# Optimization experiments

Measured on AMD Instinct MI355X. Metric: run time of the kernel, lower is better.

The kernel has to match this reference:

```python
import jax, jax.numpy as jnp
import numpy as np

B, H, E, V = 128, 1024, 1024, 40000
L, S, A = 256, 10, 10
L_S, L_A = 1.0, 1.0  # s_copy_lambda / a_copy_lambda
NEG = -1e24


def setup_inputs():
    key = jax.random.key(0)
    ks = jax.random.split(key, 32)
    n = lambda i, shape: jax.random.normal(ks[i], shape, dtype=jnp.float32)
    p = lambda i, shape: jax.random.normal(ks[i], shape, dtype=jnp.float32) * 0.02
    rnn_in = 3 * E + H  # embed + history ctx (H) + state ctx (E) + action ctx (E)
    return {
        "inp": n(0, (B, 1, E)),
        "hidden": n(1, (1, B, H)),
        "hs_vectors": n(2, (B, L, H)),
        "state_gumbel_prob": jax.random.uniform(ks[3], (B, S, V), dtype=jnp.float32),
        "state_gumbel_embed": n(4, (B, S, E)),
        "action_gumbel_prob": jax.random.uniform(ks[5], (B, A, V), dtype=jnp.float32),
        "action_gumbel_embed": n(6, (B, A, E)),
        "history_lens": jax.random.randint(ks[7], (B,), 1, L + 1),
        "history_word_indices": jax.random.randint(ks[8], (B, L), 0, V),
        # history word mlp-attention
        "Wq_hist": p(9, (H, H)), "bq_hist": jnp.zeros((H,), jnp.float32),
        "Wm_hist": p(10, (H, H)), "v_hist": p(11, (H,)),
        # init_s_attn / init_a_attn (query H, memory E)
        "Wq_s": p(12, (H, H)), "bq_s": jnp.zeros((H,), jnp.float32),
        "Wm_s": p(13, (E, H)), "v_s": p(14, (H,)),
        "Wq_a": p(15, (H, H)), "bq_a": jnp.zeros((H,), jnp.float32),
        "Wm_a": p(16, (E, H)), "v_a": p(17, (H,)),
        # sparse_copy_attn (memory E+1)
        "Wq_sc": p(18, (H, H)), "bq_sc": jnp.zeros((H,), jnp.float32),
        "Wm_sc": p(19, (E + 1, H)), "v_sc": p(20, (H,)),
        # GRU (torch layout: [3H, in], gate order r,z,n)
        "W_ih": p(21, (3 * H, rnn_in)), "W_hh": p(22, (3 * H, H)),
        "b_ih": jnp.zeros((3 * H,), jnp.float32), "b_hh": jnp.zeros((3 * H,), jnp.float32),
        # output projection
        "W_out": p(23, (H, V)), "b_out": jnp.zeros((V,), jnp.float32),
    }


def _mlp_scores(q, mem, Wq, bq, Wm, v):
    # q: [B,1,H], mem: [B,L,M] -> additive-attention logits [B,1,L]
    t = jnp.tanh((q @ Wq + bq) + (mem @ Wm))  # [B,L,H]
    return (t @ v)[:, None, :]


def reference(inp, hidden, hs_vectors, state_gumbel_prob, state_gumbel_embed,
              action_gumbel_prob, action_gumbel_embed, history_lens,
              history_word_indices, Wq_hist, bq_hist, Wm_hist, v_hist,
              Wq_s, bq_s, Wm_s, v_s, Wq_a, bq_a, Wm_a, v_a,
              Wq_sc, bq_sc, Wm_sc, v_sc, W_ih, W_hh, b_ih, b_hh, W_out, b_out):
    q0 = jnp.transpose(hidden, (1, 0, 2))  # [B,1,H]
    # --- history word attention (masked mlp attention) ---
    hist_scores = _mlp_scores(q0, hs_vectors, Wq_hist, bq_hist, Wm_hist, v_hist)
    valid = jnp.arange(L)[None, None, :] < history_lens[:, None, None]
    hist_scores = jnp.where(valid, hist_scores, NEG)
    c_his = jax.nn.softmax(hist_scores, axis=-1) @ hs_vectors  # [B,1,H]
    # --- init_consult over state / action gumbel embeddings ---
    sw = jax.nn.softmax(_mlp_scores(q0, state_gumbel_embed, Wq_s, bq_s, Wm_s, v_s), axis=-1)
    c_state = sw @ state_gumbel_embed  # [B,1,E]
    aw = jax.nn.softmax(_mlp_scores(q0, action_gumbel_embed, Wq_a, bq_a, Wm_a, v_a), axis=-1)
    c_action = aw @ action_gumbel_embed  # [B,1,E]
    x = jnp.concatenate([inp, c_his, c_state, c_action], axis=-1)[:, 0, :]  # [B,3E+H]
    # --- single-step GRU cell (torch semantics, gate order r,z,n) ---
    h0 = hidden[0]
    gi = x @ W_ih.T + b_ih
    gh = h0 @ W_hh.T + b_hh
    ir, iz, inn = jnp.split(gi, 3, axis=-1)
    hr, hz, hn = jnp.split(gh, 3, axis=-1)
    r = jax.nn.sigmoid(ir + hr)
    z = jax.nn.sigmoid(iz + hz)
    nact = jnp.tanh(inn + r * hn)
    h_new = (1.0 - z) * nact + z * h0  # [B,H]
    # --- vocab logits + copy logits, joint softmax ---
    gene_logits = h_new @ W_out + b_out  # [B,V]
    cq = h_new[:, None, :]
    hs_logits = jnp.einsum('bqh,blh->bql', cq, hs_vectors)[:, 0, :]  # dot attn, [B,L]
    s_tag = jnp.zeros((B, S, 1), jnp.float32)
    a_tag = jnp.ones((B, A, 1), jnp.float32)
    st_logits = _mlp_scores(cq, jnp.concatenate([state_gumbel_embed, s_tag], -1), Wq_sc, bq_sc, Wm_sc, v_sc)[:, 0, :]
    ac_logits = _mlp_scores(cq, jnp.concatenate([action_gumbel_embed, a_tag], -1), Wq_sc, bq_sc, Wm_sc, v_sc)[:, 0, :]
    all_logits = jnp.concatenate([gene_logits, hs_logits, st_logits, ac_logits], axis=-1)
    wp = jax.nn.softmax(all_logits, axis=-1)  # [B, V+L+S+A]
    gene_p = wp[:, :V]
    hs_w = wp[:, V:V + L]
    st_w = wp[:, V + L:V + L + S]
    ac_w = wp[:, V + L + S:]
    # --- copy-distribution mixing ---
    scp = jnp.einsum('bs,bsv->bv', st_w, state_gumbel_prob)
    acp = jnp.einsum('ba,bav->bv', ac_w, action_gumbel_prob)
    gene_p = gene_p + L_S * scp + L_A * acp
    copy_p = jnp.zeros((B, V), jnp.float32).at[jnp.arange(B)[:, None], history_word_indices].add(hs_w)
    out = jnp.log(gene_p + copy_p)[:, None, :]  # [B,1,V]
    return out, h_new[None]
```

## Files before the change

kernel.cpp:

```cpp
#include <hip/hip_runtime.h>
#include <stdint.h>

typedef __attribute__((ext_vector_type(4))) float f32x4;
typedef __attribute__((ext_vector_type(2))) unsigned int u32x2;
typedef __attribute__((ext_vector_type(4))) unsigned int u32x4;
typedef __attribute__((ext_vector_type(8))) short bf16x8;

#define BV (128*40000)

__device__ __forceinline__ unsigned rne_bf16(float f) {
    unsigned x = __float_as_uint(f);
    return ((x + 0x7FFFu + ((x >> 16) & 1u)) >> 16) & 0xFFFFu;
}
__device__ __forceinline__ unsigned pack2(float a, float b) {
    return rne_bf16(a) | (rne_bf16(b) << 16);
}
__device__ __forceinline__ float bf2f(unsigned u) {
    return __uint_as_float((u & 0xFFFFu) << 16);
}
__device__ __forceinline__ float sigm(float x) { return 1.0f / (1.0f + expf(-x)); }

__device__ __forceinline__ void gload16(const void* g, void* l) {
    __builtin_amdgcn_global_load_lds(
        (const __attribute__((address_space(1))) unsigned*)g,
        (__attribute__((address_space(3))) unsigned*)l, 16, 0, 0);
}

template<int EPI>
__device__ __forceinline__ void mgemm(
    const unsigned short* __restrict__ A, const unsigned short* __restrict__ Bt,
    float* __restrict__ out, const float* __restrict__ rb,
    const float* __restrict__ cb1, const float* __restrict__ cb2,
    const float* __restrict__ vvec,
    int m0, int n0, int kb, int ke, int ldk, int ldc, int rpb)
{
    __shared__ unsigned short As[2][4096];
    __shared__ unsigned short Bs[2][4096];
    const int t = threadIdx.x, lane = t & 63, wv = t >> 6;
    const int l16 = lane & 15, lq = lane >> 4;
    const int wm = wv >> 1, wn = wv & 1;

    const int srow = lane >> 2, scol = (lane & 3) << 3;
    const unsigned short* gA0 = A + (size_t)(m0 + (wv << 4) + srow) * ldk + kb + scol;
    const unsigned short* gA1 = gA0 + (size_t)64 * ldk;
    const unsigned short* gB0 = Bt + (size_t)(n0 + (wv << 4) + srow) * ldk + kb + scol;
    const unsigned short* gB1 = gB0 + (size_t)64 * ldk;
    unsigned short* lA0 = &As[0][wv << 9];
    unsigned short* lA1 = &As[0][(wv + 4) << 9];
    unsigned short* lB0 = &Bs[0][wv << 9];
    unsigned short* lB1 = &Bs[0][(wv + 4) << 9];

    f32x4 acc[4][4];
#pragma unroll
    for (int i = 0; i < 4; ++i)
#pragma unroll
        for (int j = 0; j < 4; ++j) acc[i][j] = (f32x4){0.f, 0.f, 0.f, 0.f};

    const int NS = (ke - kb) >> 5;
    gload16(gA0, lA0); gload16(gA1, lA1);
    gload16(gB0, lB0); gload16(gB1, lB1);

    for (int s = 0; s < NS; ++s) {
        __syncthreads();
        if (s + 1 < NS) {
            const int nb = (s + 1) & 1, ko = (s + 1) << 5;
            gload16(gA0 + ko, lA0 + (nb << 12)); gload16(gA1 + ko, lA1 + (nb << 12));
            gload16(gB0 + ko, lB0 + (nb << 12)); gload16(gB1 + ko, lB1 + (nb << 12));
        }
        const unsigned short* ab = As[s & 1];
        const unsigned short* bb = Bs[s & 1];
        bf16x8 af[4], bfv[4];
#pragma unroll
        for (int i = 0; i < 4; ++i)
            af[i] = *(const bf16x8*)(ab + (((wm << 6) + (i << 4) + l16) << 5) + (lq << 3));
#pragma unroll
        for (int i = 0; i < 4; ++i)
            bfv[i] = *(const bf16x8*)(bb + (((wn << 6) + (i << 4) + l16) << 5) + (lq << 3));
#pragma unroll
        for (int mf = 0; mf < 4; ++mf)
#pragma unroll
            for (int nf = 0; nf < 4; ++nf)
                acc[mf][nf] = __builtin_amdgcn_mfma_f32_16x16x32_bf16(af[mf], bfv[nf], acc[mf][nf], 0, 0, 0);
    }

    if (EPI == 1) {
#pragma unroll
        for (int mf = 0; mf < 4; ++mf) {
#pragma unroll
            for (int r = 0; r < 4; ++r) {
                int gr = m0 + (wm << 6) + (mf << 4) + (lq << 2) + r;
                const float* rbp = rb + (size_t)(gr / rpb) * 1024;
                float s = 0.0f;
#pragma unroll
                for (int nf = 0; nf < 4; ++nf) {
                    int gc = n0 + (wn << 6) + (nf << 4) + l16;
                    float xv = acc[mf][nf][r] + rbp[gc] + cb1[gc];
                    if (cb2) xv += cb2[gc];
                    s += tanhf(xv) * vvec[gc];
                }
#pragma unroll
                for (int msk = 1; msk < 16; msk <<= 1) s += __shfl_xor(s, msk, 64);
                if (l16 == 0) atomicAdd(&out[gr], s);
            }
        }
    } else {
#pragma unroll
        for (int mf = 0; mf < 4; ++mf) {
            int gr0 = m0 + (wm << 6) + (mf << 4) + (lq << 2);
#pragma unroll
            for (int nf = 0; nf < 4; ++nf) {
                int gc = n0 + (wn << 6) + (nf << 4) + l16;
#pragma unroll
                for (int r = 0; r < 4; ++r)
                    atomicAdd(&out[(size_t)(gr0 + r) * ldc + gc], acc[mf][nf][r]);
            }
        }
    }
}

__global__ __launch_bounds__(256) void k_hist2(
    const unsigned short* hs, const unsigned short* WmhT, const int* lens,
    const float* qh_h, const float* bq, const float* v, float* hsc) {
    int h = blockIdx.x;
    int p = h & 255, n = h >> 8;
    int b = p >> 1, l0 = (p & 1) << 7;
    if (lens[b] <= l0) return;
    mgemm<1>(hs, WmhT, hsc, qh_h, bq, nullptr, v, p << 7, n << 7, 0, 1024, 1024, 0, 256);
}

__global__ __launch_bounds__(256) void k_att3(
    const unsigned short* se, const unsigned short* ae,
    const unsigned short* WmsT, const unsigned short* WmaT,
    const float* qh_s, const float* qh_a, const float* bq_s, const float* bq_a,
    const float* v_s, const float* v_a, float* stsc, float* acsc) {
    if (blockIdx.z == 0)
        mgemm<1>(se, WmsT, stsc, qh_s, bq_s, nullptr, v_s, blockIdx.y * 128, blockIdx.x * 128, 0, 1024, 1024, 0, 10);
    else
        mgemm<1>(ae, WmaT, acsc, qh_a, bq_a, nullptr, v_a, blockIdx.y * 128, blockIdx.x * 128, 0, 1024, 1024, 0, 10);
}

__global__ __launch_bounds__(256) void k_stac3(
    const unsigned short* se, const unsigned short* ae, const unsigned short* WmscT,
    const float* tagrow, const float* qsc, const float* bq_sc, const float* v_sc,
    float* stlg, float* aclg) {
    if (blockIdx.z == 0)
        mgemm<1>(se, WmscT, stlg, qsc, bq_sc, nullptr, v_sc, blockIdx.y * 128, blockIdx.x * 128, 0, 1024, 1024, 0, 10);
    else
        mgemm<1>(ae, WmscT, aclg, qsc, bq_sc, tagrow, v_sc, blockIdx.y * 128, blockIdx.x * 128, 0, 1024, 1024, 0, 10);
}

__global__ __launch_bounds__(256) void k_qh4(
    const unsigned short* q0, const unsigned short* W0, const unsigned short* W1,
    const unsigned short* W2, float* o0, float* o1, float* o2) {
    const unsigned short* W = W0; float* o = o0;
    if (blockIdx.z == 1) { W = W1; o = o1; }
    if (blockIdx.z == 2) { W = W2; o = o2; }
    int kb = blockIdx.y << 8;
    mgemm<2>(q0, W, o, nullptr, nullptr, nullptr, nullptr, 0, blockIdx.x * 128, kb, kb + 256, 1024, 1024, 1);
}

__global__ __launch_bounds__(256) void k_gigh2(
    const unsigned short* xb, const unsigned short* q0,
    const unsigned short* Wih, const unsigned short* Whh, float* gi, float* gh) {
    if (blockIdx.z == 0) {
        int kb = blockIdx.y << 9;
        mgemm<2>(xb, Wih, gi, nullptr, nullptr, nullptr, nullptr, 0, blockIdx.x * 128, kb, kb + 512, 4096, 3072, 1);
    } else {
        if (blockIdx.y >= 2) return;
        int kb = blockIdx.y << 9;
        mgemm<2>(q0, Whh, gh, nullptr, nullptr, nullptr, nullptr, 0, blockIdx.x * 128, kb, kb + 512, 1024, 3072, 1);
    }
}

__global__ __launch_bounds__(256) void k_qsc2(
    const unsigned short* hnb, const unsigned short* WqscT, float* qsc) {
    int kb = blockIdx.y << 9;
    mgemm<2>(hnb, WqscT, qsc, nullptr, nullptr, nullptr, nullptr, 0, blockIdx.x * 128, kb, kb + 512, 1024, 1024, 1);
}

__global__ __launch_bounds__(256) void k_geneKN(
    const unsigned short* __restrict__ hnb, const float* __restrict__ Wout,
    float* __restrict__ out) {
    __shared__ unsigned short As[2][4096];
    __shared__ unsigned short Bs[2][4096];
    const int t = threadIdx.x, lane = t & 63, wv = t >> 6;
    const int l16 = lane & 15, lq = lane >> 4;
    const int wm = wv >> 1, wn = wv & 1;
    const int n0 = blockIdx.x << 7;
    const int kb = blockIdx.y << 9;

    const int srow = lane >> 2, scol = (lane & 3) << 3;
    const unsigned short* gA0 = hnb + (size_t)((wv << 4) + srow) * 1024 + kb + scol;
    const unsigned short* gA1 = gA0 + (size_t)64 * 1024;
    unsigned short* lA0 = &As[0][wv << 9];
    unsigned short* lA1 = &As[0][(wv + 4) << 9];

    const int bn = t & 127, kh = t >> 7;
    const bool ok = (n0 + bn) < 40000;
    const float* gB = Wout + (size_t)(kb + kh * 16) * 40000 + (n0 + bn);

    f32x4 acc[4][4];
#pragma unroll
    for (int i = 0; i < 4; ++i)
#pragma unroll
        for (int j = 0; j < 4; ++j) acc[i][j] = (f32x4){0.f, 0.f, 0.f, 0.f};

    auto stageB = [&](int buf, int ko) {
        const float* src = gB + (size_t)ko * 40000;
        float f[16];
#pragma unroll
        for (int j = 0; j < 16; ++j) f[j] = ok ? src[(size_t)j * 40000] : 0.0f;
        u32x4* d = (u32x4*)&Bs[buf][bn * 32 + kh * 16];
        d[0] = (u32x4){pack2(f[0],f[1]), pack2(f[2],f[3]), pack2(f[4],f[5]), pack2(f[6],f[7])};
        d[1] = (u32x4){pack2(f[8],f[9]), pack2(f[10],f[11]), pack2(f[12],f[13]), pack2(f[14],f[15])};
    };

    gload16(gA0, lA0); gload16(gA1, lA1); stageB(0, 0);
    for (int s = 0; s < 16; ++s) {
        __syncthreads();
        if (s + 1 < 16) {
            const int nb = (s + 1) & 1, ko = (s + 1) << 5;
            gload16(gA0 + ko, lA0 + (nb << 12)); gload16(gA1 + ko, lA1 + (nb << 12));
            stageB(nb, ko);
        }
        const unsigned short* ab = As[s & 1];
        const unsigned short* bb = Bs[s & 1];
        bf16x8 af[4], bfv[4];
#pragma unroll
        for (int i = 0; i < 4; ++i)
            af[i] = *(const bf16x8*)(ab + (((wm << 6) + (i << 4) + l16) << 5) + (lq << 3));
#pragma unroll
        for (int i = 0; i < 4; ++i)
            bfv[i] = *(const bf16x8*)(bb + (((wn << 6) + (i << 4) + l16) << 5) + (lq << 3));
#pragma unroll
        for (int mf = 0; mf < 4; ++mf)
#pragma unroll
            for (int nf = 0; nf < 4; ++nf)
                acc[mf][nf] = __builtin_amdgcn_mfma_f32_16x16x32_bf16(af[mf], bfv[nf], acc[mf][nf], 0, 0, 0);
    }
#pragma unroll
    for (int mf = 0; mf < 4; ++mf) {
        int gr0 = (wm << 6) + (mf << 4) + (lq << 2);
#pragma unroll
        for (int nf = 0; nf < 4; ++nf) {
            int gc = n0 + (wn << 6) + (nf << 4) + l16;
            if (gc < 40000) {
#pragma unroll
                for (int r = 0; r < 4; ++r)
                    atomicAdd(&out[(size_t)(gr0 + r) * 40000 + gc], acc[mf][nf][r]);
            }
        }
    }
}

__global__ __launch_bounds__(256) void k_cvt(const float* __restrict__ in,
                                             unsigned short* __restrict__ o, int n8) {
    int i = blockIdx.x * 256 + threadIdx.x;
    if (i >= n8) return;
    const f32x4* s = (const f32x4*)in + (size_t)i * 2;
    f32x4 a = s[0], b = s[1];
    ((u32x4*)o)[i] = (u32x4){pack2(a[0],a[1]), pack2(a[2],a[3]), pack2(b[0],b[1]), pack2(b[2],b[3])};
}

struct TrArgs { const float* s[8]; unsigned short* d[8]; };
__global__ __launch_bounds__(256) void k_trcvt(TrArgs a) {
    __shared__ float tile[64][65];
    const float* in = a.s[blockIdx.z];
    unsigned short* ot = a.d[blockIdx.z];
    int k0 = blockIdx.y << 6, n0 = blockIdx.x << 6;
    int tr = threadIdx.x >> 6, tc = threadIdx.x & 63;
#pragma unroll
    for (int i = 0; i < 16; ++i) {
        int r = (i << 2) + tr;
        tile[r][tc] = in[(size_t)(k0 + r) * 1024 + n0 + tc];
    }
    __syncthreads();
#pragma unroll
    for (int i = 0; i < 16; ++i) {
        int r = (i << 2) + tr;
        ot[(size_t)(n0 + r) * 1024 + k0 + tc] = (unsigned short)rne_bf16(tile[tc][r]);
    }
}

__device__ __forceinline__ void softmax10(const float* src, float* dst) {
    float m = src[0];
    for (int i = 1; i < 10; ++i) m = fmaxf(m, src[i]);
    float z = 0.f, e[10];
    for (int i = 0; i < 10; ++i) { e[i] = expf(src[i] - m); z += e[i]; }
    float iz = 1.0f / z;
    for (int i = 0; i < 10; ++i) dst[i] = e[i] * iz;
}

__global__ __launch_bounds__(256) void k_chis(
    const float* __restrict__ scores, const int* __restrict__ lens,
    const unsigned short* __restrict__ hs, unsigned short* __restrict__ xb) {
    int b = blockIdx.x, t = threadIdx.x;
    __shared__ float w[256];
    __shared__ float red[256];
    int len = lens[b];
    float s = scores[b * 256 + t];
    bool valid = t < len;
    red[t] = valid ? s : -3.0e38f;
    __syncthreads();
    for (int st = 128; st > 0; st >>= 1) { if (t < st) red[t] = fmaxf(red[t], red[t + st]); __syncthreads(); }
    float m = red[0];
    __syncthreads();
    float e = valid ? expf(s - m) : 0.0f;
    red[t] = e;
    __syncthreads();
    for (int st = 128; st > 0; st >>= 1) { if (t < st) red[t] += red[t + st]; __syncthreads(); }
    float Z = red[0];
    __syncthreads();
    w[t] = e / Z;
    __syncthreads();
    float a0 = 0.f, a1 = 0.f, a2 = 0.f, a3 = 0.f;
    for (int l = 0; l < 256; ++l) {
        float wl = w[l];
        if (wl == 0.0f) continue;
        u32x2 u = *((const u32x2*)(hs + ((size_t)b * 256 + l) * 1024) + t);
        a0 += wl * bf2f(u[0]); a1 += wl * bf2f(u[0] >> 16);
        a2 += wl * bf2f(u[1]); a3 += wl * bf2f(u[1] >> 16);
    }
    *((u32x2*)(xb + (size_t)b * 4096 + 1024) + t) = (u32x2){pack2(a0, a1), pack2(a2, a3)};
}

__global__ __launch_bounds__(256) void k_assemble(
    const float* __restrict__ inp, const float* __restrict__ st_sc, const float* __restrict__ ac_sc,
    const unsigned short* __restrict__ se, const unsigned short* __restrict__ ae,
    unsigned short* __restrict__ xb) {
    int b = blockIdx.x, t = threadIdx.x;
    __shared__ float sw[10], aw[10];
    if (t == 0) softmax10(st_sc + b * 10, sw);
    if (t == 64) softmax10(ac_sc + b * 10, aw);
    f32x4 iv = ((const f32x4*)(inp + (size_t)b * 1024))[t];
    *((u32x2*)(xb + (size_t)b * 4096) + t) = (u32x2){pack2(iv[0], iv[1]), pack2(iv[2], iv[3])};
    __syncthreads();
    float cs0=0,cs1=0,cs2=0,cs3=0, ca0=0,ca1=0,ca2=0,ca3=0;
#pragma unroll
    for (int s = 0; s < 10; ++s) {
        u32x2 us = *((const u32x2*)(se + ((size_t)b * 10 + s) * 1024) + t);
        u32x2 ua = *((const u32x2*)(ae + ((size_t)b * 10 + s) * 1024) + t);
        float ws = sw[s], wa = aw[s];
        cs0 += ws * bf2f(us[0]); cs1 += ws * bf2f(us[0] >> 16);
        cs2 += ws * bf2f(us[1]); cs3 += ws * bf2f(us[1] >> 16);
        ca0 += wa * bf2f(ua[0]); ca1 += wa * bf2f(ua[0] >> 16);
        ca2 += wa * bf2f(ua[1]); ca3 += wa * bf2f(ua[1] >> 16);
    }
    *((u32x2*)(xb + (size_t)b * 4096 + 2048) + t) = (u32x2){pack2(cs0, cs1), pack2(cs2, cs3)};
    *((u32x2*)(xb + (size_t)b * 4096 + 3072) + t) = (u32x2){pack2(ca0, ca1), pack2(ca2, ca3)};
}

__global__ __launch_bounds__(256) void k_gru(
    const float* __restrict__ gi, const float* __restrict__ gh,
    const float* __restrict__ b_ih, const float* __restrict__ b_hh,
    const float* __restrict__ h0, float* __restrict__ hnew,
    unsigned short* __restrict__ hnb) {
    int i = blockIdx.x * 256 + threadIdx.x;
    int b = i >> 10, j = i & 1023;
    const float* gib = gi + (size_t)b * 3072;
    const float* ghb = gh + (size_t)b * 3072;
    float ir = gib[j] + b_ih[j],           hr = ghb[j] + b_hh[j];
    float iz = gib[1024 + j] + b_ih[1024 + j], hz = ghb[1024 + j] + b_hh[1024 + j];
    float in = gib[2048 + j] + b_ih[2048 + j], hn = ghb[2048 + j] + b_hh[2048 + j];
    float r = sigm(ir + hr);
    float z = sigm(iz + hz);
    float n = tanhf(in + r * hn);
    float h = (1.0f - z) * n + z * h0[i];
    hnew[i] = h;
    hnb[i] = (unsigned short)rne_bf16(h);
}

__global__ __launch_bounds__(256) void k_hsl(
    const float* __restrict__ hnew, const unsigned short* __restrict__ hs,
    float* __restrict__ out) {
    int b = blockIdx.y;
    int w = threadIdx.x >> 6, lane = threadIdx.x & 63;
    int l = blockIdx.x * 4 + w;
    const f32x4* hr = (const f32x4*)(hnew + (size_t)b * 1024);
    const u32x4* vr = (const u32x4*)(hs + ((size_t)b * 256 + l) * 1024);
    float s = 0.f;
#pragma unroll
    for (int q = 0; q < 2; ++q) {
        u32x4 u = vr[lane * 2 + q];
        f32x4 h0 = hr[lane * 4 + q * 2], h1 = hr[lane * 4 + q * 2 + 1];
        s += h0[0]*bf2f(u[0]) + h0[1]*bf2f(u[0]>>16) + h0[2]*bf2f(u[1]) + h0[3]*bf2f(u[1]>>16);
        s += h1[0]*bf2f(u[2]) + h1[1]*bf2f(u[2]>>16) + h1[2]*bf2f(u[3]) + h1[3]*bf2f(u[3]>>16);
    }
    for (int msk = 1; msk < 64; msk <<= 1) s += __shfl_xor(s, msk, 64);
    if (lane == 0) out[b * 256 + l] = s;
}

__global__ __launch_bounds__(256) void k_smstats(
    const float* __restrict__ gene, const float* __restrict__ bo,
    const float* __restrict__ hsl, const float* __restrict__ stl, const float* __restrict__ acl,
    float* __restrict__ mbuf, float* __restrict__ zbuf) {
    int b = blockIdx.x, t = threadIdx.x;
    __shared__ float red[256];
    const f32x4* g4 = (const f32x4*)(gene + (size_t)b * 40000);
    const f32x4* b4 = (const f32x4*)bo;
    float mx = -3.0e38f;
    for (int i = t; i < 10000; i += 256) {
        f32x4 q = g4[i], bb = b4[i];
        mx = fmaxf(mx, fmaxf(fmaxf(q[0]+bb[0], q[1]+bb[1]), fmaxf(q[2]+bb[2], q[3]+bb[3])));
    }
    mx = fmaxf(mx, hsl[b * 256 + t]);
    if (t < 10) mx = fmaxf(mx, fmaxf(stl[b * 10 + t], acl[b * 10 + t]));
    red[t] = mx; __syncthreads();
    for (int s = 128; s > 0; s >>= 1) { if (t < s) red[t] = fmaxf(red[t], red[t + s]); __syncthreads(); }
    float m = red[0];
    __syncthreads();
    float sum = 0.f;
    for (int i = t; i < 10000; i += 256) {
        f32x4 q = g4[i], bb = b4[i];
        sum += expf(q[0]+bb[0]-m) + expf(q[1]+bb[1]-m) + expf(q[2]+bb[2]-m) + expf(q[3]+bb[3]-m);
    }
    sum += expf(hsl[b * 256 + t] - m);
    if (t < 10) sum += expf(stl[b * 10 + t] - m) + expf(acl[b * 10 + t] - m);
    red[t] = sum; __syncthreads();
    for (int s = 128; s > 0; s >>= 1) { if (t < s) red[t] += red[t + s]; __syncthreads(); }
    if (t == 0) { mbuf[b] = m; zbuf[b] = red[0]; }
}

__global__ __launch_bounds__(256) void k_scatter(
    const float* __restrict__ hsl, const float* __restrict__ mbuf, const float* __restrict__ zbuf,
    const int* __restrict__ hwi, float* __restrict__ copyp) {
    int b = blockIdx.x, l = threadIdx.x;
    float wv = expf(hsl[b * 256 + l] - mbuf[b]) / zbuf[b];
    int idx = hwi[b * 256 + l];
    atomicAdd(copyp + (size_t)b * 40000 + idx, wv);
}

__global__ __launch_bounds__(256) void k_final(
    float* __restrict__ gene_out, const float* __restrict__ bo, const float* __restrict__ copyp,
    const float* __restrict__ sprob, const float* __restrict__ aprob,
    const float* __restrict__ stl, const float* __restrict__ acl,
    const float* __restrict__ mbuf, const float* __restrict__ zbuf) {
    int b = blockIdx.y, t = threadIdx.x;
    __shared__ float sw[10], aw[10];
    float m = mbuf[b], iz = 1.0f / zbuf[b];
    if (t < 10) sw[t] = expf(stl[b * 10 + t] - m) * iz;
    if (t >= 64 && t < 74) aw[t - 64] = expf(acl[b * 10 + (t - 64)] - m) * iz;
    __syncthreads();
    int v4 = blockIdx.x * 256 + t;
    if (v4 < 10000) {
        size_t base = (size_t)b * 10000 + v4;
        f32x4 g = ((const f32x4*)gene_out)[base];
        f32x4 bb = ((const f32x4*)bo)[v4];
        f32x4 c = ((const f32x4*)copyp)[base];
        f32x4 acc;
#pragma unroll
        for (int j = 0; j < 4; ++j) acc[j] = expf(g[j] + bb[j] - m) * iz + c[j];
#pragma unroll
        for (int s = 0; s < 10; ++s) {
            f32x4 pv = ((const f32x4*)sprob)[((size_t)b * 10 + s) * 10000 + v4];
            f32x4 av = ((const f32x4*)aprob)[((size_t)b * 10 + s) * 10000 + v4];
            float ws = sw[s], wa = aw[s];
#pragma unroll
            for (int j = 0; j < 4; ++j) acc[j] += ws * pv[j] + wa * av[j];
        }
        f32x4 r;
#pragma unroll
        for (int j = 0; j < 4; ++j) r[j] = logf(acc[j]);
        ((f32x4*)gene_out)[base] = r;
    }
}

#define OFF_QH_H  0
#define OFF_QH_S  131072
#define OFF_QH_A  262144
#define OFF_QSC   393216
#define OFF_GI    524288
#define OFF_GH    917504
#define OFF_HSC   1310720
#define OFF_STSC  1343488
#define OFF_ACSC  1344768
#define OFF_STLG  1346048
#define OFF_ACLG  1347328
#define ZERO_FLOATS 1348608
#define OFF_HSL   1348608
#define OFF_M     1381376
#define OFF_Z     1381504
#define OFF_COPY  1381632
#define FLOAT_TOTAL 6501632
#define SO_HS     0
#define SO_SE     33554432
#define SO_AE     34865152
#define SO_Q0     36175872
#define SO_X      36306944
#define SO_HNB    36831232
#define SO_WQHT   36962304
#define SO_WQST   38010880
#define SO_WQAT   39059456
#define SO_WQSCT  40108032
#define SO_WMHT   41156608
#define SO_WMST   42205184
#define SO_WMAT   43253760
#define SO_WMSCT  44302336
#define SO_WIH    45350912
#define SO_WHH    57933824

extern "C" void kernel_launch(void* const* d_in, const int* in_sizes, int n_in,
                              void* d_out, int out_size, void* d_ws, size_t ws_size,
                              hipStream_t stream) {
    const float* inp     = (const float*)d_in[0];
    const float* hidden  = (const float*)d_in[1];
    const float* hs      = (const float*)d_in[2];
    const float* sprob   = (const float*)d_in[3];
    const float* se      = (const float*)d_in[4];
    const float* aprob   = (const float*)d_in[5];
    const float* ae      = (const float*)d_in[6];
    const int*   lens    = (const int*)d_in[7];
    const int*   hwi     = (const int*)d_in[8];
    const float* Wq_hist = (const float*)d_in[9];
    const float* bq_hist = (const float*)d_in[10];
    const float* Wm_hist = (const float*)d_in[11];
    const float* v_hist  = (const float*)d_in[12];
    const float* Wq_s    = (const float*)d_in[13];
    const float* bq_s    = (const float*)d_in[14];
    const float* Wm_s    = (const float*)d_in[15];
    const float* v_s     = (const float*)d_in[16];
    const float* Wq_a    = (const float*)d_in[17];
    const float* bq_a    = (const float*)d_in[18];
    const float* Wm_a    = (const float*)d_in[19];
    const float* v_a     = (const float*)d_in[20];
    const float* Wq_sc   = (const float*)d_in[21];
    const float* bq_sc   = (const float*)d_in[22];
    const float* Wm_sc   = (const float*)d_in[23];
    const float* v_sc    = (const float*)d_in[24];
    const float* W_ih    = (const float*)d_in[25];
    const float* W_hh    = (const float*)d_in[26];
    const float* b_ih    = (const float*)d_in[27];
    const float* b_hh    = (const float*)d_in[28];
    const float* W_out   = (const float*)d_in[29];
    const float* b_out   = (const float*)d_in[30];

    float* out  = (float*)d_out;
    float* w    = (float*)d_ws;
    float* hnew = out + BV;
    unsigned short* sb = (unsigned short*)(w + FLOAT_TOTAL);

    float* qh_h = w + OFF_QH_H;  float* qh_s = w + OFF_QH_S;  float* qh_a = w + OFF_QH_A;
    float* qsc  = w + OFF_QSC;   float* gi   = w + OFF_GI;    float* gh   = w + OFF_GH;
    float* hsc  = w + OFF_HSC;   float* stsc = w + OFF_STSC;  float* acsc = w + OFF_ACSC;
    float* stlg = w + OFF_STLG;  float* aclg = w + OFF_ACLG;
    float* hsl  = w + OFF_HSL;   float* mbuf = w + OFF_M;     float* zbuf = w + OFF_Z;
    float* copyp = w + OFF_COPY;

    unsigned short* hs_bf = sb + SO_HS;   unsigned short* se_bf = sb + SO_SE;
    unsigned short* ae_bf = sb + SO_AE;   unsigned short* q0_bf = sb + SO_Q0;
    unsigned short* x_bf  = sb + SO_X;    unsigned short* hnb   = sb + SO_HNB;
    unsigned short* WqhT  = sb + SO_WQHT; unsigned short* WqsT  = sb + SO_WQST;
    unsigned short* WqaT  = sb + SO_WQAT; unsigned short* WqscT = sb + SO_WQSCT;
    unsigned short* WmhT  = sb + SO_WMHT; unsigned short* WmsT  = sb + SO_WMST;
    unsigned short* WmaT  = sb + SO_WMAT; unsigned short* WmscT = sb + SO_WMSCT;
    unsigned short* WihB  = sb + SO_WIH;  unsigned short* WhhB  = sb + SO_WHH;

    dim3 blk(256);

    hipMemsetAsync(w, 0, (size_t)ZERO_FLOATS * 4, stream);
    hipMemsetAsync(copyp, 0, (size_t)BV * 4, stream);
    hipMemsetAsync(out, 0, (size_t)BV * 4, stream);

    k_cvt<<<dim3(16384), blk, 0, stream>>>(hs, hs_bf, 4194304);
    k_cvt<<<dim3(640),   blk, 0, stream>>>(se, se_bf, 163840);
    k_cvt<<<dim3(640),   blk, 0, stream>>>(ae, ae_bf, 163840);
    k_cvt<<<dim3(64),    blk, 0, stream>>>(hidden, q0_bf, 16384);
    k_cvt<<<dim3(6144),  blk, 0, stream>>>(W_ih, WihB, 1572864);
    k_cvt<<<dim3(1536),  blk, 0, stream>>>(W_hh, WhhB, 393216);
    TrArgs ta;
    ta.s[0]=Wq_hist; ta.s[1]=Wq_s; ta.s[2]=Wq_a; ta.s[3]=Wq_sc;
    ta.s[4]=Wm_hist; ta.s[5]=Wm_s; ta.s[6]=Wm_a; ta.s[7]=Wm_sc;
    ta.d[0]=WqhT; ta.d[1]=WqsT; ta.d[2]=WqaT; ta.d[3]=WqscT;
    ta.d[4]=WmhT; ta.d[5]=WmsT; ta.d[6]=WmaT; ta.d[7]=WmscT;
    k_trcvt<<<dim3(16, 16, 8), blk, 0, stream>>>(ta);

    k_qh4<<<dim3(8, 4, 3), blk, 0, stream>>>(q0_bf, WqhT, WqsT, WqaT, qh_h, qh_s, qh_a);
    k_hist2<<<dim3(2048), blk, 0, stream>>>(hs_bf, WmhT, lens, qh_h, bq_hist, v_hist, hsc);
    k_att3<<<dim3(8, 10, 2), blk, 0, stream>>>(se_bf, ae_bf, WmsT, WmaT, qh_s, qh_a, bq_s, bq_a, v_s, v_a, stsc, acsc);
    k_chis<<<dim3(128), blk, 0, stream>>>(hsc, lens, hs_bf, x_bf);
    k_assemble<<<dim3(128), blk, 0, stream>>>(inp, stsc, acsc, se_bf, ae_bf, x_bf);
    k_gigh2<<<dim3(24, 8, 2), blk, 0, stream>>>(x_bf, q0_bf, WihB, WhhB, gi, gh);
    k_gru<<<dim3(512), blk, 0, stream>>>(gi, gh, b_ih, b_hh, hidden, hnew, hnb);
    k_qsc2<<<dim3(8, 2), blk, 0, stream>>>(hnb, WqscT, qsc);
    k_geneKN<<<dim3(313, 2), blk, 0, stream>>>(hnb, W_out, out);
    k_hsl<<<dim3(64, 128), blk, 0, stream>>>(hnew, hs_bf, hsl);
    k_stac3<<<dim3(8, 10, 2), blk, 0, stream>>>(se_bf, ae_bf, WmscT, Wm_sc + (size_t)1024 * 1024, qsc, bq_sc, v_sc, stlg, aclg);
    k_smstats<<<dim3(128), blk, 0, stream>>>(out, b_out, hsl, stlg, aclg, mbuf, zbuf);
    k_scatter<<<dim3(128), blk, 0, stream>>>(hsl, mbuf, zbuf, hwi, copyp);
    k_final<<<dim3(40, 128), blk, 0, stream>>>(out, b_out, copyp, sprob, aprob, stlg, aclg, mbuf, zbuf);

    (void)in_sizes; (void)n_in; (void)out_size; (void)ws_size;
}
```

Baseline: 652.7 us.

## Merge kernels across pipeline and drop split-K atomics in output projection

Six conversion launches become one grid-stride kernel, and the history and state/action attention GEMMs share one launch. The context and assembly kernels are merged, as are GRU with the history dot-logits, the qsc GEMM with the output projection, and softmax stats with the copy scatter. The output projection now runs the full K=1024 per block with direct stores plus fused bias, so the output memset and atomics go away. The cost is half as many projection blocks (329 vs 626) with twice the K loop each, which may underfill the GPU.

```diff
diff --git a/kernel.cpp b/kernel.cpp
--- a/kernel.cpp
+++ b/kernel.cpp
@@ -118,25 +118,103 @@
     }
 }
 
-__global__ __launch_bounds__(256) void k_hist2(
+__device__ __forceinline__ void gene_body(
+    const unsigned short* __restrict__ hnb, const float* __restrict__ Wout,
+    const float* __restrict__ b_out, float* __restrict__ out, int n0)
+{
+    __shared__ unsigned short As[2][4096];
+    __shared__ unsigned short Bs[2][4096];
+    const int t = threadIdx.x, lane = t & 63, wv = t >> 6;
+    const int l16 = lane & 15, lq = lane >> 4;
+    const int wm = wv >> 1, wn = wv & 1;
+
+    const int srow = lane >> 2, scol = (lane & 3) << 3;
+    const unsigned short* gA0 = hnb + (size_t)((wv << 4) + srow) * 1024 + scol;
+    const unsigned short* gA1 = gA0 + (size_t)64 * 1024;
+    unsigned short* lA0 = &As[0][wv << 9];
+    unsigned short* lA1 = &As[0][(wv + 4) << 9];
+
+    const int bn = t & 127, kh = t >> 7;
+    const bool ok = (n0 + bn) < 40000;
+    const float* gB = Wout + (size_t)(kh * 16) * 40000 + (n0 + bn);
+
+    f32x4 acc[4][4];
+#pragma unroll
+    for (int i = 0; i < 4; ++i)
+#pragma unroll
+        for (int j = 0; j < 4; ++j) acc[i][j] = (f32x4){0.f, 0.f, 0.f, 0.f};
+
+    auto stageB = [&](int buf, int ko) {
+        const float* src = gB + (size_t)ko * 40000;
+        float f[16];
+#pragma unroll
+        for (int j = 0; j < 16; ++j) f[j] = ok ? src[(size_t)j * 40000] : 0.0f;
+        u32x4* d = (u32x4*)&Bs[buf][bn * 32 + kh * 16];
+        d[0] = (u32x4){pack2(f[0],f[1]), pack2(f[2],f[3]), pack2(f[4],f[5]), pack2(f[6],f[7])};
+        d[1] = (u32x4){pack2(f[8],f[9]), pack2(f[10],f[11]), pack2(f[12],f[13]), pack2(f[14],f[15])};
+    };
+
+    gload16(gA0, lA0); gload16(gA1, lA1); stageB(0, 0);
+    for (int s = 0; s < 32; ++s) {
+        __syncthreads();
+        if (s + 1 < 32) {
+            const int nb = (s + 1) & 1, ko = (s + 1) << 5;
+            gload16(gA0 + ko, lA0 + (nb << 12)); gload16(gA1 + ko, lA1 + (nb << 12));
+            stageB(nb, ko);
+        }
+        const unsigned short* ab = As[s & 1];
+        const unsigned short* bb = Bs[s & 1];
+        bf16x8 af[4], bfv[4];
+#pragma unroll
+        for (int i = 0; i < 4; ++i)
+            af[i] = *(const bf16x8*)(ab + (((wm << 6) + (i << 4) + l16) << 5) + (lq << 3));
+#pragma unroll
+        for (int i = 0; i < 4; ++i)
+            bfv[i] = *(const bf16x8*)(bb + (((wn << 6) + (i << 4) + l16) << 5) + (lq << 3));
+#pragma unroll
+        for (int mf = 0; mf < 4; ++mf)
+#pragma unroll
+            for (int nf = 0; nf < 4; ++nf)
+                acc[mf][nf] = __builtin_amdgcn_mfma_f32_16x16x32_bf16(af[mf], bfv[nf], acc[mf][nf], 0, 0, 0);
+    }
+#pragma unroll
+    for (int mf = 0; mf < 4; ++mf) {
+        int gr0 = (wm << 6) + (mf << 4) + (lq << 2);
+#pragma unroll
+        for (int nf = 0; nf < 4; ++nf) {
+            int gc = n0 + (wn << 6) + (nf << 4) + l16;
+            if (gc < 40000) {
+                float bo = b_out[gc];
+#pragma unroll
+                for (int r = 0; r < 4; ++r)
+                    out[(size_t)(gr0 + r) * 40000 + gc] = acc[mf][nf][r] + bo;
+            }
+        }
+    }
+}
+
+__global__ __launch_bounds__(256) void k_hist_att(
     const unsigned short* hs, const unsigned short* WmhT, const int* lens,
-    const float* qh_h, const float* bq, const float* v, float* hsc) {
-    int h = blockIdx.x;
-    int p = h & 255, n = h >> 8;
-    int b = p >> 1, l0 = (p & 1) << 7;
-    if (lens[b] <= l0) return;
-    mgemm<1>(hs, WmhT, hsc, qh_h, bq, nullptr, v, p << 7, n << 7, 0, 1024, 1024, 0, 256);
-}
-
-__global__ __launch_bounds__(256) void k_att3(
+    const float* qh_h, const float* bq_h, const float* v_h, float* hsc,
     const unsigned short* se, const unsigned short* ae,
     const unsigned short* WmsT, const unsigned short* WmaT,
     const float* qh_s, const float* qh_a, const float* bq_s, const float* bq_a,
     const float* v_s, const float* v_a, float* stsc, float* acsc) {
-    if (blockIdx.z == 0)
-        mgemm<1>(se, WmsT, stsc, qh_s, bq_s, nullptr, v_s, blockIdx.y * 128, blockIdx.x * 128, 0, 1024, 1024, 0, 10);
-    else
-        mgemm<1>(ae, WmaT, acsc, qh_a, bq_a, nullptr, v_a, blockIdx.y * 128, blockIdx.x * 128, 0, 1024, 1024, 0, 10);
+    int id = blockIdx.x;
+    if (id < 2048) {
+        int p = id & 255, n = id >> 8;
+        int b = p >> 1, l0 = (p & 1) << 7;
+        if (lens[b] <= l0) return;
+        mgemm<1>(hs, WmhT, hsc, qh_h, bq_h, nullptr, v_h, p << 7, n << 7, 0, 1024, 1024, 0, 256);
+    } else {
+        int r = id - 2048;
+        int z = r / 80; r -= z * 80;
+        int y = r >> 3, x = r & 7;
+        if (z == 0)
+            mgemm<1>(se, WmsT, stsc, qh_s, bq_s, nullptr, v_s, y * 128, x * 128, 0, 1024, 1024, 0, 10);
+        else
+            mgemm<1>(ae, WmaT, acsc, qh_a, bq_a, nullptr, v_a, y * 128, x * 128, 0, 1024, 1024, 0, 10);
+    }
 }
 
 __global__ __launch_bounds__(256) void k_stac3(
@@ -172,94 +250,30 @@
     }
 }
 
-__global__ __launch_bounds__(256) void k_qsc2(
-    const unsigned short* hnb, const unsigned short* WqscT, float* qsc) {
-    int kb = blockIdx.y << 9;
-    mgemm<2>(hnb, WqscT, qsc, nullptr, nullptr, nullptr, nullptr, 0, blockIdx.x * 128, kb, kb + 512, 1024, 1024, 1);
-}
-
-__global__ __launch_bounds__(256) void k_geneKN(
-    const unsigned short* __restrict__ hnb, const float* __restrict__ Wout,
-    float* __restrict__ out) {
-    __shared__ unsigned short As[2][4096];
-    __shared__ unsigned short Bs[2][4096];
-    const int t = threadIdx.x, lane = t & 63, wv = t >> 6;
-    const int l16 = lane & 15, lq = lane >> 4;
-    const int wm = wv >> 1, wn = wv & 1;
-    const int n0 = blockIdx.x << 7;
-    const int kb = blockIdx.y << 9;
-
-    const int srow = lane >> 2, scol = (lane & 3) << 3;
-    const unsigned short* gA0 = hnb + (size_t)((wv << 4) + srow) * 1024 + kb + scol;
-    const unsigned short* gA1 = gA0 + (size_t)64 * 1024;
-    unsigned short* lA0 = &As[0][wv << 9];
-    unsigned short* lA1 = &As[0][(wv + 4) << 9];
-
-    const int bn = t & 127, kh = t >> 7;
-    const bool ok = (n0 + bn) < 40000;
-    const float* gB = Wout + (size_t)(kb + kh * 16) * 40000 + (n0 + bn);
-
-    f32x4 acc[4][4];
-#pragma unroll
-    for (int i = 0; i < 4; ++i)
-#pragma unroll
-        for (int j = 0; j < 4; ++j) acc[i][j] = (f32x4){0.f, 0.f, 0.f, 0.f};
-
-    auto stageB = [&](int buf, int ko) {
-        const float* src = gB + (size_t)ko * 40000;
-        float f[16];
-#pragma unroll
-        for (int j = 0; j < 16; ++j) f[j] = ok ? src[(size_t)j * 40000] : 0.0f;
-        u32x4* d = (u32x4*)&Bs[buf][bn * 32 + kh * 16];
-        d[0] = (u32x4){pack2(f[0],f[1]), pack2(f[2],f[3]), pack2(f[4],f[5]), pack2(f[6],f[7])};
-        d[1] = (u32x4){pack2(f[8],f[9]), pack2(f[10],f[11]), pack2(f[12],f[13]), pack2(f[14],f[15])};
-    };
-
-    gload16(gA0, lA0); gload16(gA1, lA1); stageB(0, 0);
-    for (int s = 0; s < 16; ++s) {
-        __syncthreads();
-        if (s + 1 < 16) {
-            const int nb = (s + 1) & 1, ko = (s + 1) << 5;
-            gload16(gA0 + ko, lA0 + (nb << 12)); gload16(gA1 + ko, lA1 + (nb << 12));
-            stageB(nb, ko);
-        }
-        const unsigned short* ab = As[s & 1];
-        const unsigned short* bb = Bs[s & 1];
-        bf16x8 af[4], bfv[4];
-#pragma unroll
-        for (int i = 0; i < 4; ++i)
-            af[i] = *(const bf16x8*)(ab + (((wm << 6) + (i << 4) + l16) << 5) + (lq << 3));
-#pragma unroll
-        for (int i = 0; i < 4; ++i)
-            bfv[i] = *(const bf16x8*)(bb + (((wn << 6) + (i << 4) + l16) << 5) + (lq << 3));
-#pragma unroll
-        for (int mf = 0; mf < 4; ++mf)
-#pragma unroll
-            for (int nf = 0; nf < 4; ++nf)
-                acc[mf][nf] = __builtin_amdgcn_mfma_f32_16x16x32_bf16(af[mf], bfv[nf], acc[mf][nf], 0, 0, 0);
-    }
-#pragma unroll
-    for (int mf = 0; mf < 4; ++mf) {
-        int gr0 = (wm << 6) + (mf << 4) + (lq << 2);
-#pragma unroll
-        for (int nf = 0; nf < 4; ++nf) {
-            int gc = n0 + (wn << 6) + (nf << 4) + l16;
-            if (gc < 40000) {
-#pragma unroll
-                for (int r = 0; r < 4; ++r)
-                    atomicAdd(&out[(size_t)(gr0 + r) * 40000 + gc], acc[mf][nf][r]);
-            }
-        }
-    }
-}
-
-__global__ __launch_bounds__(256) void k_cvt(const float* __restrict__ in,
-                                             unsigned short* __restrict__ o, int n8) {
-    int i = blockIdx.x * 256 + threadIdx.x;
-    if (i >= n8) return;
-    const f32x4* s = (const f32x4*)in + (size_t)i * 2;
-    f32x4 a = s[0], b = s[1];
-    ((u32x4*)o)[i] = (u32x4){pack2(a[0],a[1]), pack2(a[2],a[3]), pack2(b[0],b[1]), pack2(b[2],b[3])};
+__global__ __launch_bounds__(256) void k_qsc_gene(
+    const unsigned short* hnb, const unsigned short* WqscT, float* qsc,
+    const float* Wout, const float* b_out, float* out) {
+    int id = blockIdx.x;
+    if (id < 16) {
+        int x = id & 7, kb = (id >> 3) << 9;
+        mgemm<2>(hnb, WqscT, qsc, nullptr, nullptr, nullptr, nullptr, 0, x * 128, kb, kb + 512, 1024, 1024, 1);
+    } else {
+        gene_body(hnb, Wout, b_out, out, (id - 16) << 7);
+    }
+}
+
+struct CvtArgs { const float* s[6]; unsigned short* d[6]; int pre[7]; };
+__global__ __launch_bounds__(256) void k_cvt_all(CvtArgs a) {
+    int total = a.pre[6];
+    for (int i = blockIdx.x * 256 + threadIdx.x; i < total; i += gridDim.x * 256) {
+        int seg = 0;
+        while (i >= a.pre[seg + 1]) ++seg;
+        int loc = i - a.pre[seg];
+        const f32x4* s4 = (const f32x4*)a.s[seg] + (size_t)loc * 2;
+        f32x4 q0 = s4[0], q1 = s4[1];
+        ((u32x4*)a.d[seg])[loc] =
+            (u32x4){pack2(q0[0],q0[1]), pack2(q0[2],q0[3]), pack2(q1[0],q1[1]), pack2(q1[2],q1[3])};
+    }
 }
 
 struct TrArgs { const float* s[8]; unsigned short* d[8]; };
@@ -291,12 +305,16 @@
     for (int i = 0; i < 10; ++i) dst[i] = e[i] * iz;
 }
 
-__global__ __launch_bounds__(256) void k_chis(
+__global__ __launch_bounds__(256) void k_ctx(
     const float* __restrict__ scores, const int* __restrict__ lens,
-    const unsigned short* __restrict__ hs, unsigned short* __restrict__ xb) {
+    const unsigned short* __restrict__ hs,
+    const float* __restrict__ inp, const float* __restrict__ st_sc, const float* __restrict__ ac_sc,
+    const unsigned short* __restrict__ se, const unsigned short* __restrict__ ae,
+    unsigned short* __restrict__ xb) {
     int b = blockIdx.x, t = threadIdx.x;
     __shared__ float w[256];
     __shared__ float red[256];
+    __shared__ float sw[10], aw[10];
     int len = lens[b];
     float s = scores[b * 256 + t];
     bool valid = t < len;
@@ -312,6 +330,10 @@
     float Z = red[0];
     __syncthreads();
     w[t] = e / Z;
+    if (t == 0) softmax10(st_sc + b * 10, sw);
+    if (t == 64) softmax10(ac_sc + b * 10, aw);
+    f32x4 iv = ((const f32x4*)(inp + (size_t)b * 1024))[t];
+    *((u32x2*)(xb + (size_t)b * 4096) + t) = (u32x2){pack2(iv[0], iv[1]), pack2(iv[2], iv[3])};
     __syncthreads();
     float a0 = 0.f, a1 = 0.f, a2 = 0.f, a3 = 0.f;
     for (int l = 0; l < 256; ++l) {
@@ -322,25 +344,12 @@
         a2 += wl * bf2f(u[1]); a3 += wl * bf2f(u[1] >> 16);
     }
     *((u32x2*)(xb + (size_t)b * 4096 + 1024) + t) = (u32x2){pack2(a0, a1), pack2(a2, a3)};
-}
-
-__global__ __launch_bounds__(256) void k_assemble(
-    const float* __restrict__ inp, const float* __restrict__ st_sc, const float* __restrict__ ac_sc,
-    const unsigned short* __restrict__ se, const unsigned short* __restrict__ ae,
-    unsigned short* __restrict__ xb) {
-    int b = blockIdx.x, t = threadIdx.x;
-    __shared__ float sw[10], aw[10];
-    if (t == 0) softmax10(st_sc + b * 10, sw);
-    if (t == 64) softmax10(ac_sc + b * 10, aw);
-    f32x4 iv = ((const f32x4*)(inp + (size_t)b * 1024))[t];
-    *((u32x2*)(xb + (size_t)b * 4096) + t) = (u32x2){pack2(iv[0], iv[1]), pack2(iv[2], iv[3])};
-    __syncthreads();
     float cs0=0,cs1=0,cs2=0,cs3=0, ca0=0,ca1=0,ca2=0,ca3=0;
 #pragma unroll
-    for (int s = 0; s < 10; ++s) {
-        u32x2 us = *((const u32x2*)(se + ((size_t)b * 10 + s) * 1024) + t);
-        u32x2 ua = *((const u32x2*)(ae + ((size_t)b * 10 + s) * 1024) + t);
-        float ws = sw[s], wa = aw[s];
+    for (int q = 0; q < 10; ++q) {
+        u32x2 us = *((const u32x2*)(se + ((size_t)b * 10 + q) * 1024) + t);
+        u32x2 ua = *((const u32x2*)(ae + ((size_t)b * 10 + q) * 1024) + t);
+        float ws = sw[q], wa = aw[q];
         cs0 += ws * bf2f(us[0]); cs1 += ws * bf2f(us[0] >> 16);
         cs2 += ws * bf2f(us[1]); cs3 += ws * bf2f(us[1] >> 16);
         ca0 += wa * bf2f(ua[0]); ca1 += wa * bf2f(ua[0] >> 16);
@@ -350,60 +359,58 @@
     *((u32x2*)(xb + (size_t)b * 4096 + 3072) + t) = (u32x2){pack2(ca0, ca1), pack2(ca2, ca3)};
 }
 
-__global__ __launch_bounds__(256) void k_gru(
+__global__ __launch_bounds__(1024) void k_gruhsl(
     const float* __restrict__ gi, const float* __restrict__ gh,
     const float* __restrict__ b_ih, const float* __restrict__ b_hh,
     const float* __restrict__ h0, float* __restrict__ hnew,
-    unsigned short* __restrict__ hnb) {
-    int i = blockIdx.x * 256 + threadIdx.x;
-    int b = i >> 10, j = i & 1023;
+    unsigned short* __restrict__ hnb,
+    const unsigned short* __restrict__ hs, float* __restrict__ hsl) {
+    int b = blockIdx.x, j = threadIdx.x;
+    size_t i = (size_t)b * 1024 + j;
     const float* gib = gi + (size_t)b * 3072;
     const float* ghb = gh + (size_t)b * 3072;
-    float ir = gib[j] + b_ih[j],           hr = ghb[j] + b_hh[j];
-    float iz = gib[1024 + j] + b_ih[1024 + j], hz = ghb[1024 + j] + b_hh[1024 + j];
-    float in = gib[2048 + j] + b_ih[2048 + j], hn = ghb[2048 + j] + b_hh[2048 + j];
-    float r = sigm(ir + hr);
-    float z = sigm(iz + hz);
-    float n = tanhf(in + r * hn);
+    float r = sigm(gib[j] + b_ih[j] + ghb[j] + b_hh[j]);
+    float z = sigm(gib[1024 + j] + b_ih[1024 + j] + ghb[1024 + j] + b_hh[1024 + j]);
+    float hn = ghb[2048 + j] + b_hh[2048 + j];
+    float n = tanhf(gib[2048 + j] + b_ih[2048 + j] + r * hn);
     float h = (1.0f - z) * n + z * h0[i];
     hnew[i] = h;
     hnb[i] = (unsigned short)rne_bf16(h);
-}
-
-__global__ __launch_bounds__(256) void k_hsl(
-    const float* __restrict__ hnew, const unsigned short* __restrict__ hs,
-    float* __restrict__ out) {
-    int b = blockIdx.y;
-    int w = threadIdx.x >> 6, lane = threadIdx.x & 63;
-    int l = blockIdx.x * 4 + w;
-    const f32x4* hr = (const f32x4*)(hnew + (size_t)b * 1024);
-    const u32x4* vr = (const u32x4*)(hs + ((size_t)b * 256 + l) * 1024);
-    float s = 0.f;
-#pragma unroll
-    for (int q = 0; q < 2; ++q) {
-        u32x4 u = vr[lane * 2 + q];
-        f32x4 h0 = hr[lane * 4 + q * 2], h1 = hr[lane * 4 + q * 2 + 1];
-        s += h0[0]*bf2f(u[0]) + h0[1]*bf2f(u[0]>>16) + h0[2]*bf2f(u[1]) + h0[3]*bf2f(u[1]>>16);
-        s += h1[0]*bf2f(u[2]) + h1[1]*bf2f(u[2]>>16) + h1[2]*bf2f(u[3]) + h1[3]*bf2f(u[3]>>16);
-    }
-    for (int msk = 1; msk < 64; msk <<= 1) s += __shfl_xor(s, msk, 64);
-    if (lane == 0) out[b * 256 + l] = s;
-}
-
-__global__ __launch_bounds__(256) void k_smstats(
-    const float* __restrict__ gene, const float* __restrict__ bo,
-    const float* __restrict__ hsl, const float* __restrict__ stl, const float* __restrict__ acl,
-    float* __restrict__ mbuf, float* __restrict__ zbuf) {
+    __shared__ float hsm[1024];
+    hsm[j] = h;
+    __syncthreads();
+    int wave = j >> 6, lane = j & 63;
+    float hr[16];
+#pragma unroll
+    for (int k = 0; k < 16; ++k) hr[k] = hsm[lane * 16 + k];
+    for (int l = wave; l < 256; l += 16) {
+        const u32x4* row = (const u32x4*)(hs + ((size_t)b * 256 + l) * 1024);
+        u32x4 u0 = row[lane * 2], u1 = row[lane * 2 + 1];
+        float s = hr[0]*bf2f(u0[0]) + hr[1]*bf2f(u0[0]>>16) + hr[2]*bf2f(u0[1]) + hr[3]*bf2f(u0[1]>>16)
+                + hr[4]*bf2f(u0[2]) + hr[5]*bf2f(u0[2]>>16) + hr[6]*bf2f(u0[3]) + hr[7]*bf2f(u0[3]>>16)
+                + hr[8]*bf2f(u1[0]) + hr[9]*bf2f(u1[0]>>16) + hr[10]*bf2f(u1[1]) + hr[11]*bf2f(u1[1]>>16)
+                + hr[12]*bf2f(u1[2]) + hr[13]*bf2f(u1[2]>>16) + hr[14]*bf2f(u1[3]) + hr[15]*bf2f(u1[3]>>16);
+#pragma unroll
+        for (int msk = 1; msk < 64; msk <<= 1) s += __shfl_xor(s, msk, 64);
+        if (lane == 0) hsl[b * 256 + l] = s;
+    }
+}
+
+__global__ __launch_bounds__(256) void k_smsc(
+    const float* __restrict__ gene, const float* __restrict__ hsl,
+    const float* __restrict__ stl, const float* __restrict__ acl,
+    const int* __restrict__ hwi,
+    float* __restrict__ mbuf, float* __restrict__ zbuf, float* __restrict__ copyp) {
     int b = blockIdx.x, t = threadIdx.x;
     __shared__ float red[256];
     const f32x4* g4 = (const f32x4*)(gene + (size_t)b * 40000);
-    const f32x4* b4 = (const f32x4*)bo;
     float mx = -3.0e38f;
     for (int i = t; i < 10000; i += 256) {
-        f32x4 q = g4[i], bb = b4[i];
-        mx = fmaxf(mx, fmaxf(fmaxf(q[0]+bb[0], q[1]+bb[1]), fmaxf(q[2]+bb[2], q[3]+bb[3])));
-    }
-    mx = fmaxf(mx, hsl[b * 256 + t]);
+        f32x4 q = g4[i];
+        mx = fmaxf(mx, fmaxf(fmaxf(q[0], q[1]), fmaxf(q[2], q[3])));
+    }
+    float hv = hsl[b * 256 + t];
+    mx = fmaxf(mx, hv);
     if (t < 10) mx = fmaxf(mx, fmaxf(stl[b * 10 + t], acl[b * 10 + t]));
     red[t] = mx; __syncthreads();
     for (int s = 128; s > 0; s >>= 1) { if (t < s) red[t] = fmaxf(red[t], red[t + s]); __syncthreads(); }
@@ -411,27 +418,21 @@
     __syncthreads();
     float sum = 0.f;
     for (int i = t; i < 10000; i += 256) {
-        f32x4 q = g4[i], bb = b4[i];
-        sum += expf(q[0]+bb[0]-m) + expf(q[1]+bb[1]-m) + expf(q[2]+bb[2]-m) + expf(q[3]+bb[3]-m);
-    }
-    sum += expf(hsl[b * 256 + t] - m);
+        f32x4 q = g4[i];
+        sum += expf(q[0]-m) + expf(q[1]-m) + expf(q[2]-m) + expf(q[3]-m);
+    }
+    sum += expf(hv - m);
     if (t < 10) sum += expf(stl[b * 10 + t] - m) + expf(acl[b * 10 + t] - m);
     red[t] = sum; __syncthreads();
     for (int s = 128; s > 0; s >>= 1) { if (t < s) red[t] += red[t + s]; __syncthreads(); }
-    if (t == 0) { mbuf[b] = m; zbuf[b] = red[0]; }
-}
-
-__global__ __launch_bounds__(256) void k_scatter(
-    const float* __restrict__ hsl, const float* __restrict__ mbuf, const float* __restrict__ zbuf,
-    const int* __restrict__ hwi, float* __restrict__ copyp) {
-    int b = blockIdx.x, l = threadIdx.x;
-    float wv = expf(hsl[b * 256 + l] - mbuf[b]) / zbuf[b];
-    int idx = hwi[b * 256 + l];
-    atomicAdd(copyp + (size_t)b * 40000 + idx, wv);
+    float Z = red[0];
+    if (t == 0) { mbuf[b] = m; zbuf[b] = Z; }
+    float wv = expf(hv - m) / Z;
+    atomicAdd(copyp + (size_t)b * 40000 + hwi[b * 256 + t], wv);
 }
 
 __global__ __launch_bounds__(256) void k_final(
-    float* __restrict__ gene_out, const float* __restrict__ bo, const float* __restrict__ copyp,
+    float* __restrict__ gene_out, const float* __restrict__ copyp,
     const float* __restrict__ sprob, const float* __restrict__ aprob,
     const float* __restrict__ stl, const float* __restrict__ acl,
     const float* __restrict__ mbuf, const float* __restrict__ zbuf) {
@@ -445,11 +446,10 @@
     if (v4 < 10000) {
         size_t base = (size_t)b * 10000 + v4;
         f32x4 g = ((const f32x4*)gene_out)[base];
-        f32x4 bb = ((const f32x4*)bo)[v4];
         f32x4 c = ((const f32x4*)copyp)[base];
         f32x4 acc;
 #pragma unroll
-        for (int j = 0; j < 4; ++j) acc[j] = expf(g[j] + bb[j] - m) * iz + c[j];
+        for (int j = 0; j < 4; ++j) acc[j] = expf(g[j] - m) * iz + c[j];
 #pragma unroll
         for (int s = 0; s < 10; ++s) {
             f32x4 pv = ((const f32x4*)sprob)[((size_t)b * 10 + s) * 10000 + v4];
@@ -559,14 +559,14 @@
 
     hipMemsetAsync(w, 0, (size_t)ZERO_FLOATS * 4, stream);
     hipMemsetAsync(copyp, 0, (size_t)BV * 4, stream);
-    hipMemsetAsync(out, 0, (size_t)BV * 4, stream);
-
-    k_cvt<<<dim3(16384), blk, 0, stream>>>(hs, hs_bf, 4194304);
-    k_cvt<<<dim3(640),   blk, 0, stream>>>(se, se_bf, 163840);
-    k_cvt<<<dim3(640),   blk, 0, stream>>>(ae, ae_bf, 163840);
-    k_cvt<<<dim3(64),    blk, 0, stream>>>(hidden, q0_bf, 16384);
-    k_cvt<<<dim3(6144),  blk, 0, stream>>>(W_ih, WihB, 1572864);
-    k_cvt<<<dim3(1536),  blk, 0, stream>>>(W_hh, WhhB, 393216);
+
+    CvtArgs ca;
+    ca.s[0]=hs; ca.s[1]=se; ca.s[2]=ae; ca.s[3]=hidden; ca.s[4]=W_ih; ca.s[5]=W_hh;
+    ca.d[0]=hs_bf; ca.d[1]=se_bf; ca.d[2]=ae_bf; ca.d[3]=q0_bf; ca.d[4]=WihB; ca.d[5]=WhhB;
+    ca.pre[0]=0; ca.pre[1]=4194304; ca.pre[2]=4358144; ca.pre[3]=4521984;
+    ca.pre[4]=4538368; ca.pre[5]=6111232; ca.pre[6]=6504448;
+    k_cvt_all<<<dim3(4096), blk, 0, stream>>>(ca);
+
     TrArgs ta;
     ta.s[0]=Wq_hist; ta.s[1]=Wq_s; ta.s[2]=Wq_a; ta.s[3]=Wq_sc;
     ta.s[4]=Wm_hist; ta.s[5]=Wm_s; ta.s[6]=Wm_a; ta.s[7]=Wm_sc;
@@ -575,19 +575,17 @@
     k_trcvt<<<dim3(16, 16, 8), blk, 0, stream>>>(ta);
 
     k_qh4<<<dim3(8, 4, 3), blk, 0, stream>>>(q0_bf, WqhT, WqsT, WqaT, qh_h, qh_s, qh_a);
-    k_hist2<<<dim3(2048), blk, 0, stream>>>(hs_bf, WmhT, lens, qh_h, bq_hist, v_hist, hsc);
-    k_att3<<<dim3(8, 10, 2), blk, 0, stream>>>(se_bf, ae_bf, WmsT, WmaT, qh_s, qh_a, bq_s, bq_a, v_s, v_a, stsc, acsc);
-    k_chis<<<dim3(128), blk, 0, stream>>>(hsc, lens, hs_bf, x_bf);
-    k_assemble<<<dim3(128), blk, 0, stream>>>(inp, stsc, acsc, se_bf, ae_bf, x_bf);
+    k_hist_att<<<dim3(2208), blk, 0, stream>>>(hs_bf, WmhT, lens, qh_h, bq_hist, v_hist, hsc,
+                                               se_bf, ae_bf, WmsT, WmaT, qh_s, qh_a, bq_s, bq_a,
+                                               v_s, v_a, stsc, acsc);
+    k_ctx<<<dim3(128), blk, 0, stream>>>(hsc, lens, hs_bf, inp, stsc, acsc, se_bf, ae_bf, x_bf);
     k_gigh2<<<dim3(24, 8, 2), blk, 0, stream>>>(x_bf, q0_bf, WihB, WhhB, gi, gh);
-    k_gru<<<dim3(512), blk, 0, stream>>>(gi, gh, b_ih, b_hh, hidden, hnew, hnb);
-    k_qsc2<<<dim3(8, 2), blk, 0, stream>>>(hnb, WqscT, qsc);
-    k_geneKN<<<dim3(313, 2), blk, 0, stream>>>(hnb, W_out, out);
-    k_hsl<<<dim3(64, 128), blk, 0, stream>>>(hnew, hs_bf, hsl);
-    k_stac3<<<dim3(8, 10, 2), blk, 0, stream>>>(se_bf, ae_bf, WmscT, Wm_sc + (size_t)1024 * 1024, qsc, bq_sc, v_sc, stlg, aclg);
-    k_smstats<<<dim3(128), blk, 0, stream>>>(out, b_out, hsl, stlg, aclg, mbuf, zbuf);
-    k_scatter<<<dim3(128), blk, 0, stream>>>(hsl, mbuf, zbuf, hwi, copyp);
-    k_final<<<dim3(40, 128), blk, 0, stream>>>(out, b_out, copyp, sprob, aprob, stlg, aclg, mbuf, zbuf);
+    k_gruhsl<<<dim3(128), dim3(1024), 0, stream>>>(gi, gh, b_ih, b_hh, hidden, hnew, hnb, hs_bf, hsl);
+    k_qsc_gene<<<dim3(329), blk, 0, stream>>>(hnb, WqscT, qsc, W_out, b_out, out);
+    k_stac3<<<dim3(8, 10, 2), blk, 0, stream>>>(se_bf, ae_bf, WmscT, Wm_sc + (size_t)1024 * 1024,
+                                                qsc, bq_sc, v_sc, stlg, aclg);
+    k_smsc<<<dim3(128), blk, 0, stream>>>(out, hsl, stlg, aclg, hwi, mbuf, zbuf, copyp);
+    k_final<<<dim3(40, 128), blk, 0, stream>>>(out, copyp, sprob, aprob, stlg, aclg, mbuf, zbuf);
 
     (void)in_sizes; (void)n_in; (void)out_size; (void)ws_size;
 }
```

Result: faster. 591.2 us (-9.4%).
